# Performance work log

Hardware: AMD Instinct MI355X
Metric: run time of the kernel (lower is better)

The kernel has to match this reference:

```python
import jax, jax.numpy as jnp
import numpy as np

N, E = 100000, 1600000
HID, N_CHUNKS, STRU = 128, 8, 4


def setup_inputs() -> dict:
    key = jax.random.key(0)
    ks = jax.random.split(key, 7)
    x = jax.random.normal(ks[0], (N, HID), dtype=jnp.float32)
    e = jax.random.randint(ks[1], (2, E), 0, N, dtype=jnp.int64)
    ratio = jax.random.uniform(ks[2], (), dtype=jnp.float32)
    out_w = N_CHUNKS * STRU
    Wq = jax.random.normal(ks[3], (out_w, HID), dtype=jnp.float32) / np.sqrt(HID)
    bq = jax.random.normal(ks[4], (out_w,), dtype=jnp.float32) * 0.01
    Wv = jax.random.normal(ks[5], (out_w, HID), dtype=jnp.float32) / np.sqrt(HID)
    bv = jax.random.normal(ks[6], (out_w,), dtype=jnp.float32) * 0.01
    return {"x": x, "e": e, "ratio": ratio, "Wq": Wq, "bq": bq, "Wv": Wv, "bv": bv}


def reference(x, e, ratio, Wq, bq, Wv, bv):
    # edge-indexed gather of endpoint features: [E, HID]
    eu = x[e[0]]
    ev = x[e[1]]
    # two linear projections, elementwise multiply: [E, STRU*N_CHUNKS]
    ku = eu @ Wq.T + bq
    kv = ev @ Wv.T + bv
    ks = ku * kv
    # hsplit(STRU) -> STRU contiguous chunks of width N_CHUNKS; sum each chunk
    sums = ks.reshape(E, STRU, N_CHUNKS).sum(axis=-1)  # [E, STRU]
    w = jax.nn.sigmoid(sums) * (1.0 - ratio) * 0.5 + 1.0
    # original returns a list of STRU arrays of shape [E]; stack for a single output
    return jnp.transpose(w)  # [STRU, E]
```

## Files before the change

kernel.cpp:

```cpp
#include <hip/hip_runtime.h>
#include <hip/hip_bf16.h>
#include <cstddef>

constexpr int HID  = 128;
constexpr int OUTW = 32;
constexpr int TOT  = 64;
constexpr int STRU = 4;
constexpr int NCH  = 8;

typedef short  bf16x8 __attribute__((ext_vector_type(8)));
typedef float  f32x4  __attribute__((ext_vector_type(4)));
typedef int    int4v  __attribute__((ext_vector_type(4)));
typedef unsigned short u16x8 __attribute__((ext_vector_type(8)));

__device__ __forceinline__ unsigned short f2bf(float f) {
    unsigned u = __builtin_bit_cast(unsigned, f);
    u += 0x7FFFu + ((u >> 16) & 1u);
    return (unsigned short)(u >> 16);
}

__device__ __forceinline__ float dot4(float4 a, float4 b) {
    return a.x * b.x + a.y * b.y + a.z * b.z + a.w * b.w;
}

__device__ __forceinline__ float bfdot(int4v a, int4v b, float sum) {
#pragma unroll
    for (int w = 0; w < 4; ++w) {
        float alo = __builtin_bit_cast(float, (unsigned)(a[w] << 16));
        float ahi = __builtin_bit_cast(float, (unsigned)a[w] & 0xffff0000u);
        float blo = __builtin_bit_cast(float, (unsigned)(b[w] << 16));
        float bhi = __builtin_bit_cast(float, (unsigned)b[w] & 0xffff0000u);
        sum = fmaf(alo, blo, sum);
        sum = fmaf(ahi, bhi, sum);
    }
    return sum;
}

__global__ __launch_bounds__(256) void proj_mfma(
    const float* __restrict__ x,
    const float* __restrict__ Wq, const float* __restrict__ bq,
    const float* __restrict__ Wv, const float* __restrict__ bv,
    unsigned short* __restrict__ P,
    unsigned short* __restrict__ Q,
    int n_nodes)
{
    __shared__ unsigned short sW[TOT * HID];
    __shared__ unsigned short sPQ[64][TOT + 8];

    const int tid  = threadIdx.x;
    const int wid  = tid >> 6;
    const int lane = tid & 63;
    const int lr   = lane & 15;
    const int lg   = lane >> 4;

    const int bases[2] = { (int)blockIdx.x * 64,
                           (int)(blockIdx.x + gridDim.x) * 64 };

    f32x4 xv[2][8];
#pragma unroll
    for (int it = 0; it < 2; ++it) {
        const int  arow = bases[it] + wid * 16 + lr;
        const bool aok  = arow < n_nodes;
        const float* ap = x + (size_t)arow * HID;
#pragma unroll
        for (int kc = 0; kc < 4; ++kc) {
            if (aok) {
                const f32x4* p = reinterpret_cast<const f32x4*>(ap + kc * 32 + lg * 8);
                xv[it][2 * kc + 0] = p[0];
                xv[it][2 * kc + 1] = p[1];
            } else {
                xv[it][2 * kc + 0] = (f32x4)0.f;
                xv[it][2 * kc + 1] = (f32x4)0.f;
            }
        }
    }

#pragma unroll
    for (int g = 0; g < 4; ++g) {
        int f     = tid * 8 + g * 2048;
        int lane6 = (f >> 3) & 63;
        int kc    = (f >> 9) & 3;
        int t     = f >> 11;
        int o     = t * 16 + (lane6 & 15);
        int k0    = kc * 32 + (lane6 >> 4) * 8;
        const float* wrow = (o < OUTW) ? (Wq + (size_t)o * HID)
                                       : (Wv + (size_t)(o - OUTW) * HID);
        f32x4 w0 = *reinterpret_cast<const f32x4*>(wrow + k0);
        f32x4 w1 = *reinterpret_cast<const f32x4*>(wrow + k0 + 4);
        u16x8 pk;
        pk[0] = f2bf(w0[0]); pk[1] = f2bf(w0[1]); pk[2] = f2bf(w0[2]); pk[3] = f2bf(w0[3]);
        pk[4] = f2bf(w1[0]); pk[5] = f2bf(w1[1]); pk[6] = f2bf(w1[2]); pk[7] = f2bf(w1[3]);
        *reinterpret_cast<u16x8*>(sW + f) = pk;
    }

    __syncthreads();

#pragma unroll
    for (int it = 0; it < 2; ++it) {
        const int base = bases[it];

        f32x4 acc[4];
#pragma unroll
        for (int t = 0; t < 4; ++t) {
            float b = (t < 2) ? bq[t * 16 + lr] : bv[(t - 2) * 16 + lr];
            acc[t][0] = b; acc[t][1] = b; acc[t][2] = b; acc[t][3] = b;
        }

#pragma unroll
        for (int kc = 0; kc < 4; ++kc) {
            f32x4 f0 = xv[it][2 * kc + 0], f1 = xv[it][2 * kc + 1];
            bf16x8 a;
            a[0] = (short)f2bf(f0[0]); a[1] = (short)f2bf(f0[1]);
            a[2] = (short)f2bf(f0[2]); a[3] = (short)f2bf(f0[3]);
            a[4] = (short)f2bf(f1[0]); a[5] = (short)f2bf(f1[1]);
            a[6] = (short)f2bf(f1[2]); a[7] = (short)f2bf(f1[3]);
#pragma unroll
            for (int t = 0; t < 4; ++t) {
                bf16x8 bf = *reinterpret_cast<const bf16x8*>(
                    sW + ((size_t)(t * 4 + kc) * 64 + lane) * 8);
                acc[t] = __builtin_amdgcn_mfma_f32_16x16x32_bf16(a, bf, acc[t], 0, 0, 0);
            }
        }

        if (it) __syncthreads();

        const int lrow = wid * 16 + lg * 4;
#pragma unroll
        for (int t = 0; t < 4; ++t)
#pragma unroll
            for (int j = 0; j < 4; ++j)
                sPQ[lrow + j][t * 16 + lr] = f2bf(acc[t][j]);
        __syncthreads();

        const int row  = tid >> 2;
        const int q    = tid & 3;
        const int node = base + row;
        if (node < n_nodes) {
            const int scol = q * 16;
            u16x8 v0 = *reinterpret_cast<const u16x8*>(&sPQ[row][scol]);
            u16x8 v1 = *reinterpret_cast<const u16x8*>(&sPQ[row][scol + 8]);
            unsigned short* dstbase = (q < 2) ? (P + (size_t)node * OUTW + q * 16)
                                              : (Q + (size_t)node * OUTW + (q - 2) * 16);
            u16x8* dst = reinterpret_cast<u16x8*>(dstbase);
            dst[0] = v0;
            dst[1] = v1;
        }
    }
}

__global__ __launch_bounds__(256) void edge_bf16(
    const int* __restrict__ e,
    const unsigned short* __restrict__ P,
    const unsigned short* __restrict__ Q,
    const float* __restrict__ ratio_p,
    float* __restrict__ out, int E_)
{
    int i = blockIdx.x * blockDim.x + threadIdx.x;
    if (i >= E_) return;

    float scale = (1.0f - ratio_p[0]) * 0.5f;
    int e0 = __builtin_nontemporal_load(e + i);
    int e1 = __builtin_nontemporal_load(e + E_ + i);

    const int4v* p4 = reinterpret_cast<const int4v*>(P + (size_t)e0 * OUTW);
    const int4v* q4 = reinterpret_cast<const int4v*>(Q + (size_t)e1 * OUTW);

    int4v a[STRU], b[STRU];
#pragma unroll
    for (int s = 0; s < STRU; ++s) { a[s] = p4[s]; b[s] = q4[s]; }

#pragma unroll
    for (int s = 0; s < STRU; ++s) {
        float sum = bfdot(a[s], b[s], 0.f);
        float sig = 1.0f / (1.0f + __expf(-sum));
        float r   = sig * scale + 1.0f;
        __builtin_nontemporal_store(r, out + (size_t)s * E_ + i);
    }
}

__global__ __launch_bounds__(256) void fused_kernel(
    const float* __restrict__ x,
    const int* __restrict__ e,
    const float* __restrict__ ratio_p,
    const float* __restrict__ Wq, const float* __restrict__ bq,
    const float* __restrict__ Wv, const float* __restrict__ bv,
    float* __restrict__ out, int E_)
{
    int i = blockIdx.x * blockDim.x + threadIdx.x;
    if (i >= E_) return;

    float scale = (1.0f - ratio_p[0]) * 0.5f;
    int e0 = e[i];
    int e1 = e[E_ + i];

    const float4* __restrict__ xu  = reinterpret_cast<const float4*>(x + (size_t)e0 * HID);
    const float4* __restrict__ xv_ = reinterpret_cast<const float4*>(x + (size_t)e1 * HID);
    const float4* __restrict__ Wq4 = reinterpret_cast<const float4*>(Wq);
    const float4* __restrict__ Wv4 = reinterpret_cast<const float4*>(Wv);

#pragma unroll 1
    for (int s = 0; s < STRU; ++s) {
        float accP[NCH], accQ[NCH];
#pragma unroll
        for (int c = 0; c < NCH; ++c) { accP[c] = bq[s*NCH+c]; accQ[c] = bv[s*NCH+c]; }
        for (int kc = 0; kc < HID / 4; ++kc) {
            float4 u = xu[kc];
            float4 v = xv_[kc];
#pragma unroll
            for (int c = 0; c < NCH; ++c) {
                int o = s * NCH + c;
                accP[c] += dot4(u, Wq4[o * (HID / 4) + kc]);
                accQ[c] += dot4(v, Wv4[o * (HID / 4) + kc]);
            }
        }
        float sum = 0.0f;
#pragma unroll
        for (int c = 0; c < NCH; ++c) sum += accP[c] * accQ[c];
        float sig = 1.0f / (1.0f + __expf(-sum));
        out[(size_t)s * E_ + i] = sig * scale + 1.0f;
    }
}

extern "C" void kernel_launch(void* const* d_in, const int* in_sizes, int n_in,
                              void* d_out, int out_size, void* d_ws, size_t ws_size,
                              hipStream_t stream)
{
    const float* x     = (const float*)d_in[0];
    const int*   e     = (const int*)  d_in[1];
    const float* ratio = (const float*)d_in[2];
    const float* Wq    = (const float*)d_in[3];
    const float* bq    = (const float*)d_in[4];
    const float* Wv    = (const float*)d_in[5];
    const float* bv    = (const float*)d_in[6];
    float* out = (float*)d_out;

    int N_ = in_sizes[0] / HID;
    int E_ = in_sizes[1] / 2;

    size_t need = (size_t)N_ * OUTW * 2 * sizeof(unsigned short);
    if (ws_size >= need) {
        unsigned short* P  = (unsigned short*)d_ws;
        unsigned short* Qb = P + (size_t)N_ * OUTW;

        int ntiles = (N_ + 63) / 64;
        int grid   = (ntiles + 1) / 2;
        proj_mfma<<<grid, 256, 0, stream>>>(x, Wq, bq, Wv, bv, P, Qb, N_);
        edge_bf16<<<(E_ + 255) / 256, 256, 0, stream>>>(e, P, Qb, ratio, out, E_);
    } else {
        fused_kernel<<<(E_ + 255) / 256, 256, 0, stream>>>(x, e, ratio, Wq, bq, Wv, bv, out, E_);
    }
}
```

Baseline: 67.30 us.

## Stage x tile through padded LDS with coalesced loads, one tile per block

The projection kernel now loads its 64-row x tile with fully coalesced float4 loads into a padded shared-memory buffer, replacing per-lane strided register loads. The MFMA A operands are then read from LDS. Each block handles one tile instead of two, which doubles the grid, and the output staging buffer reuses the x buffer. The aim is better global load coalescing and more blocks in flight. The cost is larger LDS use per block (about 49KB), which may limit occupancy, plus an extra barrier and a pass through LDS.

```diff
diff --git a/kernel.cpp b/kernel.cpp
--- a/kernel.cpp
+++ b/kernel.cpp
@@ -7,6 +7,7 @@
 constexpr int TOT  = 64;
 constexpr int STRU = 4;
 constexpr int NCH  = 8;
+constexpr int RPAD = 132;
 
 typedef short  bf16x8 __attribute__((ext_vector_type(8)));
 typedef float  f32x4  __attribute__((ext_vector_type(4)));
@@ -45,33 +46,26 @@
     int n_nodes)
 {
     __shared__ unsigned short sW[TOT * HID];
-    __shared__ unsigned short sPQ[64][TOT + 8];
+    __shared__ float sX[64 * RPAD];
 
     const int tid  = threadIdx.x;
     const int wid  = tid >> 6;
     const int lane = tid & 63;
     const int lr   = lane & 15;
     const int lg   = lane >> 4;
-
-    const int bases[2] = { (int)blockIdx.x * 64,
-                           (int)(blockIdx.x + gridDim.x) * 64 };
-
-    f32x4 xv[2][8];
-#pragma unroll
-    for (int it = 0; it < 2; ++it) {
-        const int  arow = bases[it] + wid * 16 + lr;
-        const bool aok  = arow < n_nodes;
-        const float* ap = x + (size_t)arow * HID;
-#pragma unroll
-        for (int kc = 0; kc < 4; ++kc) {
-            if (aok) {
-                const f32x4* p = reinterpret_cast<const f32x4*>(ap + kc * 32 + lg * 8);
-                xv[it][2 * kc + 0] = p[0];
-                xv[it][2 * kc + 1] = p[1];
-            } else {
-                xv[it][2 * kc + 0] = (f32x4)0.f;
-                xv[it][2 * kc + 1] = (f32x4)0.f;
-            }
+    const int base = blockIdx.x * 64;
+
+    {
+        const float4* xg = reinterpret_cast<const float4*>(x + (size_t)base * HID);
+        const int rows   = (n_nodes - base < 64) ? (n_nodes - base) : 64;
+        const int maxf4  = rows * 32;
+#pragma unroll
+        for (int j = 0; j < 8; ++j) {
+            int g = tid + 256 * j;
+            float4 v = make_float4(0.f, 0.f, 0.f, 0.f);
+            if (g < maxf4) v = xg[g];
+            int row = g >> 5, c4 = g & 31;
+            *reinterpret_cast<float4*>(&sX[row * RPAD + c4 * 4]) = v;
         }
     }
 
@@ -93,58 +87,59 @@
         *reinterpret_cast<u16x8*>(sW + f) = pk;
     }
 
+    f32x4 acc[4];
+#pragma unroll
+    for (int t = 0; t < 4; ++t) {
+        float b = (t < 2) ? bq[t * 16 + lr] : bv[(t - 2) * 16 + lr];
+        acc[t][0] = b; acc[t][1] = b; acc[t][2] = b; acc[t][3] = b;
+    }
+
     __syncthreads();
 
-#pragma unroll
-    for (int it = 0; it < 2; ++it) {
-        const int base = bases[it];
-
-        f32x4 acc[4];
+    const int xrow = wid * 16 + lr;
+#pragma unroll
+    for (int kc = 0; kc < 4; ++kc) {
+        const float* xp = &sX[xrow * RPAD + kc * 32 + lg * 8];
+        f32x4 f0 = *reinterpret_cast<const f32x4*>(xp);
+        f32x4 f1 = *reinterpret_cast<const f32x4*>(xp + 4);
+        bf16x8 a;
+        a[0] = (short)f2bf(f0[0]); a[1] = (short)f2bf(f0[1]);
+        a[2] = (short)f2bf(f0[2]); a[3] = (short)f2bf(f0[3]);
+        a[4] = (short)f2bf(f1[0]); a[5] = (short)f2bf(f1[1]);
+        a[6] = (short)f2bf(f1[2]); a[7] = (short)f2bf(f1[3]);
 #pragma unroll
         for (int t = 0; t < 4; ++t) {
-            float b = (t < 2) ? bq[t * 16 + lr] : bv[(t - 2) * 16 + lr];
-            acc[t][0] = b; acc[t][1] = b; acc[t][2] = b; acc[t][3] = b;
+            bf16x8 bf = *reinterpret_cast<const bf16x8*>(
+                sW + ((size_t)(t * 4 + kc) * 64 + lane) * 8);
+            acc[t] = __builtin_amdgcn_mfma_f32_16x16x32_bf16(a, bf, acc[t], 0, 0, 0);
         }
-
-#pragma unroll
-        for (int kc = 0; kc < 4; ++kc) {
-            f32x4 f0 = xv[it][2 * kc + 0], f1 = xv[it][2 * kc + 1];
-            bf16x8 a;
-            a[0] = (short)f2bf(f0[0]); a[1] = (short)f2bf(f0[1]);
-            a[2] = (short)f2bf(f0[2]); a[3] = (short)f2bf(f0[3]);
-            a[4] = (short)f2bf(f1[0]); a[5] = (short)f2bf(f1[1]);
-            a[6] = (short)f2bf(f1[2]); a[7] = (short)f2bf(f1[3]);
-#pragma unroll
-            for (int t = 0; t < 4; ++t) {
-                bf16x8 bf = *reinterpret_cast<const bf16x8*>(
-                    sW + ((size_t)(t * 4 + kc) * 64 + lane) * 8);
-                acc[t] = __builtin_amdgcn_mfma_f32_16x16x32_bf16(a, bf, acc[t], 0, 0, 0);
-            }
-        }
-
-        if (it) __syncthreads();
-
-        const int lrow = wid * 16 + lg * 4;
-#pragma unroll
-        for (int t = 0; t < 4; ++t)
-#pragma unroll
-            for (int j = 0; j < 4; ++j)
-                sPQ[lrow + j][t * 16 + lr] = f2bf(acc[t][j]);
-        __syncthreads();
-
-        const int row  = tid >> 2;
-        const int q    = tid & 3;
-        const int node = base + row;
-        if (node < n_nodes) {
-            const int scol = q * 16;
-            u16x8 v0 = *reinterpret_cast<const u16x8*>(&sPQ[row][scol]);
-            u16x8 v1 = *reinterpret_cast<const u16x8*>(&sPQ[row][scol + 8]);
-            unsigned short* dstbase = (q < 2) ? (P + (size_t)node * OUTW + q * 16)
-                                              : (Q + (size_t)node * OUTW + (q - 2) * 16);
-            u16x8* dst = reinterpret_cast<u16x8*>(dstbase);
-            dst[0] = v0;
-            dst[1] = v1;
-        }
+    }
+
+    __syncthreads();
+
+    unsigned short (*sPQ)[TOT + 8] =
+        reinterpret_cast<unsigned short (*)[TOT + 8]>(sX);
+
+    const int lrow = wid * 16 + lg * 4;
+#pragma unroll
+    for (int t = 0; t < 4; ++t)
+#pragma unroll
+        for (int j = 0; j < 4; ++j)
+            sPQ[lrow + j][t * 16 + lr] = f2bf(acc[t][j]);
+    __syncthreads();
+
+    const int row  = tid >> 2;
+    const int q    = tid & 3;
+    const int node = base + row;
+    if (node < n_nodes) {
+        const int scol = q * 16;
+        u16x8 v0 = *reinterpret_cast<const u16x8*>(&sPQ[row][scol]);
+        u16x8 v1 = *reinterpret_cast<const u16x8*>(&sPQ[row][scol + 8]);
+        unsigned short* dstbase = (q < 2) ? (P + (size_t)node * OUTW + q * 16)
+                                          : (Q + (size_t)node * OUTW + (q - 2) * 16);
+        u16x8* dst = reinterpret_cast<u16x8*>(dstbase);
+        dst[0] = v0;
+        dst[1] = v1;
     }
 }
 
@@ -242,9 +237,7 @@
         unsigned short* P  = (unsigned short*)d_ws;
         unsigned short* Qb = P + (size_t)N_ * OUTW;
 
-        int ntiles = (N_ + 63) / 64;
-        int grid   = (ntiles + 1) / 2;
-        proj_mfma<<<grid, 256, 0, stream>>>(x, Wq, bq, Wv, bv, P, Qb, N_);
+        proj_mfma<<<(N_ + 63) / 64, 256, 0, stream>>>(x, Wq, bq, Wv, bv, P, Qb, N_);
         edge_bf16<<<(E_ + 255) / 256, 256, 0, stream>>>(e, P, Qb, ratio, out, E_);
     } else {
         fused_kernel<<<(E_ + 255) / 256, 256, 0, stream>>>(x, e, ratio, Wq, bq, Wv, bv, out, E_);
```

After: 70.14 us. 1.04x slower.
